# Kernel tuning notes

Hardware: AMD Instinct MI355X
Metric: run time of the kernel (lower is better)

## Reference

```python
import jax, jax.numpy as jnp
import numpy as np

NUM_HEADS = 16


def _rope_tables(seq_len, head_dim, dtype=jnp.float32):
    inv_freq = 1.0 / (10000.0 ** (jnp.arange(0, head_dim, 2, dtype=jnp.float32) / head_dim))
    t = jnp.arange(seq_len, dtype=jnp.float32)
    freqs = jnp.einsum('i,j->ij', t, inv_freq)            # [s, d/2]
    emb = jnp.concatenate([freqs, freqs], axis=-1)        # [s, d]
    return emb.astype(dtype).cos if False else (jnp.cos(emb).astype(dtype), jnp.sin(emb).astype(dtype))


def _rotate_half(x):
    x1, x2 = jnp.split(x, 2, axis=-1)
    return jnp.concatenate([-x2, x1], axis=-1)


def setup_inputs() -> dict:
    key = jax.random.key(0)
    ks = jax.random.split(key, 5)
    B, S, H = 32, 256, 2048
    hidden_states = jax.random.normal(ks[0], (B, S, H), dtype=jnp.float32)
    scale = 1.0 / np.sqrt(H)
    Wq = jax.random.normal(ks[1], (H, H), dtype=jnp.float32) * scale
    Wk = jax.random.normal(ks[2], (H, H), dtype=jnp.float32) * scale
    Wv = jax.random.normal(ks[3], (H, H), dtype=jnp.float32) * scale
    Wo = jax.random.normal(ks[4], (H, H), dtype=jnp.float32) * scale
    return {"hidden_states": hidden_states, "Wq": Wq, "Wk": Wk, "Wv": Wv, "Wo": Wo}


def reference(hidden_states, Wq, Wk, Wv, Wo):
    B, S, H = hidden_states.shape
    nh = NUM_HEADS
    hd = H // nh
    scale = hd ** (-0.5)

    # projections (nn.Linear: x @ W.T, no bias)
    q = hidden_states @ Wq.T
    k = hidden_states @ Wk.T
    v = hidden_states @ Wv.T

    # b s (h d) -> b h s d
    q = q.reshape(B, S, nh, hd).transpose(0, 2, 1, 3)
    k = k.reshape(B, S, nh, hd).transpose(0, 2, 1, 3)
    v = v.reshape(B, S, nh, hd).transpose(0, 2, 1, 3)

    cos, sin = _rope_tables(S, hd, hidden_states.dtype)   # [s, hd]
    cos = cos[None, None]                                  # [1,1,s,hd]
    sin = sin[None, None]
    q = q * cos + _rotate_half(q) * sin
    k = k * cos + _rotate_half(k) * sin

    attn = jnp.einsum('bhqd,bhkd->bhqk', q, k) * scale
    attn = jax.nn.softmax(attn, axis=-1)
    out = jnp.einsum('bhqk,bhkd->bhqd', attn, v)

    out = out.transpose(0, 2, 1, 3).reshape(B, S, H)       # b h s d -> b s (h d)
    return out @ Wo.T
```

## Files before the change

kernel.cpp:

```cpp
#include <hip/hip_runtime.h>
#include <math.h>

#define B_ 32
#define S_ 256
#define H_ 2048
#define NH_ 16
#define HD_ 128
#define M_ (B_*S_)
#define K_ H_

typedef unsigned short u16;
typedef unsigned int   u32;
typedef _Float16 half8 __attribute__((ext_vector_type(8)));
typedef __attribute__((ext_vector_type(8))) unsigned short ushort8;
typedef __attribute__((ext_vector_type(4))) float  floatx4;

typedef __attribute__((address_space(3))) u32 lds_u32;
typedef __attribute__((address_space(1))) const u32 glb_u32;

__device__ __forceinline__ u16 f2h(float f) {
    _Float16 h = (_Float16)f;
    u16 r; __builtin_memcpy(&r, &h, 2); return r;
}
__device__ __forceinline__ float h2f(u16 u) {
    _Float16 h; __builtin_memcpy(&h, &u, 2); return (float)h;
}
__device__ __forceinline__ void gll16(const u16* g, u16* l) {
    __builtin_amdgcn_global_load_lds((glb_u32*)g, (lds_u32*)l, 16, 0, 0);
}

__global__ __launch_bounds__(256) void cvt16(const float* __restrict__ x,
    u16* __restrict__ o, int n4)
{
    int i = blockIdx.x * 256 + threadIdx.x;
    if (i >= n4) return;
    float4 v = ((const float4*)x)[i];
    ((ushort4*)o)[i] = make_ushort4(f2h(v.x), f2h(v.y), f2h(v.z), f2h(v.w));
}

__global__ __launch_bounds__(512, 2) void gemm_f16(
    const u16* __restrict__ A, const u16* __restrict__ Bm,
    void* __restrict__ outv, int mode)
{
    __shared__ u16 sA[2][8192], sB[2][8192];

    const int tid  = threadIdx.x;
    const int lane = tid & 63, w = tid >> 6;
    const int wm   = w >> 2, wn = w & 3;
    const int r15  = lane & 15, quad = lane >> 4;

    const int bid = blockIdx.x;
    const int swz = (bid & 7) * 32 + (bid >> 3);
    const int bx  = swz & 7;
    const int by  = swz >> 3;

    const int srow = tid & 255;
    const int c0   = tid >> 8;
    const u16* gA = A  + (size_t)(by*256 + srow) * K_ + c0*8;
    const u16* gB = Bm + (size_t)(bx*256 + srow) * K_ + c0*8;
    const int segE = w * 512;
    const int segO = 4096 + w * 512;

    const int aBase = (quad*256 + wm*128 + r15) * 8;
    const int bBase = (quad*256 + wn*64  + r15) * 8;

    const floatx4 fzero = {0.f, 0.f, 0.f, 0.f};
    floatx4 acc[8][4];
#pragma unroll
    for (int mi = 0; mi < 8; ++mi)
#pragma unroll
        for (int ni = 0; ni < 4; ++ni) acc[mi][ni] = fzero;

#define STAGE4(nbuf) do {                                                   \
        gll16(gA,      &sA[nbuf][segE]); gll16(gA + 16, &sA[nbuf][segO]);   \
        gll16(gB,      &sB[nbuf][segE]); gll16(gB + 16, &sB[nbuf][segO]);   \
        gA += 32; gB += 32; } while (0)

    STAGE4(0);
    STAGE4(1);
    asm volatile("s_waitcnt vmcnt(4)" ::: "memory");
    __builtin_amdgcn_s_barrier();

    const int NT = K_/32;
    int cur = 0;
    for (int kt = 0; kt < NT; ++kt) {
        half8 a[8], b[4];
#pragma unroll
        for (int mi = 0; mi < 8; ++mi)
            a[mi] = *(const half8*)&sA[cur][aBase + mi*128];
#pragma unroll
        for (int ni = 0; ni < 4; ++ni)
            b[ni] = *(const half8*)&sB[cur][bBase + ni*128];

        __builtin_amdgcn_s_setprio(1);
#pragma unroll
        for (int mi = 0; mi < 4; ++mi)
#pragma unroll
            for (int ni = 0; ni < 4; ++ni)
                acc[mi][ni] = __builtin_amdgcn_mfma_f32_16x16x32_f16(a[mi], b[ni], acc[mi][ni], 0, 0, 0);
        __builtin_amdgcn_s_setprio(0);

        asm volatile("s_waitcnt lgkmcnt(0)" ::: "memory");
        __builtin_amdgcn_sched_barrier(0);
        __builtin_amdgcn_s_barrier();
        __builtin_amdgcn_sched_barrier(0);
        if (kt < NT - 2) {
            STAGE4(cur);
            __builtin_amdgcn_sched_barrier(0);
        }

        __builtin_amdgcn_s_setprio(1);
#pragma unroll
        for (int mi = 4; mi < 8; ++mi)
#pragma unroll
            for (int ni = 0; ni < 4; ++ni)
                acc[mi][ni] = __builtin_amdgcn_mfma_f32_16x16x32_f16(a[mi], b[ni], acc[mi][ni], 0, 0, 0);
        __builtin_amdgcn_s_setprio(0);

        if (kt < NT - 2)       asm volatile("s_waitcnt vmcnt(4)" ::: "memory");
        else if (kt == NT - 2) asm volatile("s_waitcnt vmcnt(0)" ::: "memory");
        if (kt < NT - 1) __builtin_amdgcn_s_barrier();
        cur ^= 1;
    }
#undef STAGE4

    if (mode == 0) {
        u16* out = (u16*)outv;
#pragma unroll
        for (int mi = 0; mi < 8; ++mi)
#pragma unroll
            for (int r = 0; r < 4; ++r) {
                int m  = by*256 + wm*128 + mi*16 + quad*4 + r;
                int bb = m >> 8, ss = m & 255;
#pragma unroll
                for (int ni = 0; ni < 4; ++ni) {
                    int n = bx*256 + wn*64 + ni*16 + r15;
                    int h = n >> 7, d = n & 127;
                    out[(((size_t)(bb*NH_ + h)) * S_ + ss) * HD_ + d] = f2h(acc[mi][ni][r]);
                }
            }
    } else {
        float* out = (float*)outv;
#pragma unroll
        for (int mi = 0; mi < 8; ++mi)
#pragma unroll
            for (int r = 0; r < 4; ++r) {
                int m = by*256 + wm*128 + mi*16 + quad*4 + r;
                size_t base = (size_t)m * H_ + bx*256 + wn*64 + r15;
#pragma unroll
                for (int ni = 0; ni < 4; ++ni)
                    out[base + ni*16] = acc[mi][ni][r];
            }
    }
}

__global__ __launch_bounds__(256) void rope_f16(u16* __restrict__ q, u16* __restrict__ k)
{
    int idx = blockIdx.x * 256 + threadIdx.x;
    u16* p = blockIdx.y ? k : q;
    int i  = idx & 63;
    int s  = (idx >> 6) & (S_ - 1);
    int bh = idx >> 14;
    size_t base = ((size_t)bh * S_ + s) * HD_;
    float f = expf((float)i * -0.14391156831212788f);
    float ang = (float)s * f;
    float c = cosf(ang), sn = sinf(ang);
    float x0 = h2f(p[base + i]), x1 = h2f(p[base + i + 64]);
    p[base + i]      = f2h(x0 * c - x1 * sn);
    p[base + i + 64] = f2h(x1 * c + x0 * sn);
}

#define SCALE 0.08838834764831845f

__global__ __launch_bounds__(256) void attn_mfma(
    const u16* __restrict__ Q, const u16* __restrict__ K, const u16* __restrict__ V,
    u16* __restrict__ O)
{
    __shared__ u16 shQK[16384];
    __shared__ u16 shV[8192];
    u16* Qs = shQK;
    u16* Ks = shQK + 8192;
    u16* Pb = shQK;

    const int tid = threadIdx.x;
    const int lane = tid & 63, w = tid >> 6;
    const int r15 = lane & 15, quad = lane >> 4;
    const int bh = blockIdx.x;
    const int q0 = blockIdx.y << 6;
    const int wq = w * 16;

    const u16* Qg = Q + ((size_t)bh * S_ + q0) * HD_;
    const u16* Kg = K + (size_t)bh * S_ * HD_;
    const u16* Vg = V + (size_t)bh * S_ * HD_;

#pragma unroll
    for (int p = 0; p < 4; ++p) {
        int task = tid + (p << 8);
        int r = task & 63, c = task >> 6;
        *(uint4*)&Qs[(c*64 + r)*8] = *(const uint4*)&Qg[(size_t)r*HD_ + c*8];
    }

    const floatx4 fzero = {0.f, 0.f, 0.f, 0.f};
    floatx4 sc[4][4];
    for (int kt = 0; kt < 4; ++kt) {
        __syncthreads();
#pragma unroll
        for (int p = 0; p < 4; ++p) {
            int task = tid + (p << 8);
            int r = task & 63, c = task >> 6;
            *(uint4*)&Ks[(c*64 + r)*8] = *(const uint4*)&Kg[(size_t)(kt*64 + r)*HD_ + c*8];
        }
        __syncthreads();
#pragma unroll
        for (int ni = 0; ni < 4; ++ni) sc[kt][ni] = fzero;
#pragma unroll
        for (int ks = 0; ks < 4; ++ks) {
            half8 a = *(const half8*)&Qs[((ks*4 + quad)*64 + wq + r15)*8];
#pragma unroll
            for (int ni = 0; ni < 4; ++ni) {
                half8 b = *(const half8*)&Ks[((ks*4 + quad)*64 + ni*16 + r15)*8];
                sc[kt][ni] = __builtin_amdgcn_mfma_f32_16x16x32_f16(a, b, sc[kt][ni], 0, 0, 0);
            }
        }
    }
    __syncthreads();

#pragma unroll
    for (int kt = 0; kt < 4; ++kt)
#pragma unroll
        for (int ni = 0; ni < 4; ++ni) sc[kt][ni] *= SCALE;

    float rinv4[4], mrow4[4];
#pragma unroll
    for (int r = 0; r < 4; ++r) {
        float m = -1e30f;
#pragma unroll
        for (int kt = 0; kt < 4; ++kt)
#pragma unroll
            for (int ni = 0; ni < 4; ++ni) m = fmaxf(m, sc[kt][ni][r]);
#pragma unroll
        for (int o = 1; o < 16; o <<= 1) m = fmaxf(m, __shfl_xor(m, o));
        mrow4[r] = m;
    }
#pragma unroll
    for (int r = 0; r < 4; ++r) {
        float ssum = 0.f;
#pragma unroll
        for (int kt = 0; kt < 4; ++kt)
#pragma unroll
            for (int ni = 0; ni < 4; ++ni) {
                float e = __expf(sc[kt][ni][r] - mrow4[r]);
                sc[kt][ni][r] = e;
                ssum += e;
            }
#pragma unroll
        for (int o = 1; o < 16; o <<= 1) ssum += __shfl_xor(ssum, o);
        rinv4[r] = 1.f / ssum;
    }
#pragma unroll
    for (int r = 0; r < 4; ++r) {
        int row = wq + quad*4 + r;
#pragma unroll
        for (int kt = 0; kt < 4; ++kt)
#pragma unroll
            for (int ni = 0; ni < 4; ++ni) {
                int col = kt*64 + ni*16 + r15;
                Pb[((col >> 3)*64 + row)*8 + (col & 7)] = f2h(sc[kt][ni][r] * rinv4[r]);
            }
    }

    floatx4 oacc[8];
#pragma unroll
    for (int di = 0; di < 8; ++di) oacc[di] = fzero;

    for (int vt = 0; vt < 4; ++vt) {
        __syncthreads();
#pragma unroll
        for (int p = 0; p < 4; ++p) {
            int task = tid + (p << 8);
            int r = task & 63, dc = task >> 6;
            ushort8 v = *(const ushort8*)&Vg[(size_t)(vt*64 + r)*HD_ + dc*8];
#pragma unroll
            for (int j = 0; j < 8; ++j)
                shV[(((r >> 3)*128) + dc*8 + j)*8 + (r & 7)] = v[j];
        }
        __syncthreads();
#pragma unroll
        for (int ks = 0; ks < 2; ++ks) {
            int colbase = vt*64 + ks*32 + quad*8;
            half8 a = *(const half8*)&Pb[((colbase >> 3)*64 + wq + r15)*8];
            int sp = ks*32 + quad*8;
#pragma unroll
            for (int di = 0; di < 8; ++di) {
                half8 b = *(const half8*)&shV[((sp >> 3)*128 + di*16 + r15)*8];
                oacc[di] = __builtin_amdgcn_mfma_f32_16x16x32_f16(a, b, oacc[di], 0, 0, 0);
            }
        }
    }

    const int brow = bh >> 4, h = bh & 15;
#pragma unroll
    for (int r = 0; r < 4; ++r) {
        size_t base = ((size_t)(brow*S_ + q0 + wq + quad*4 + r)) * H_ + h*128 + r15;
#pragma unroll
        for (int di = 0; di < 8; ++di)
            O[base + di*16] = f2h(oacc[di][r]);
    }
}

extern "C" void kernel_launch(void* const* d_in, const int* in_sizes, int n_in,
                              void* d_out, int out_size, void* d_ws, size_t ws_size,
                              hipStream_t stream)
{
    const float* X  = (const float*)d_in[0];
    const float* Wp[4] = {(const float*)d_in[1], (const float*)d_in[2],
                          (const float*)d_in[3], (const float*)d_in[4]};
    float* outp = (float*)d_out;

    char* ws = (char*)d_ws;
    u16* Xh  = (u16*)ws;
    u16* W16 = (u16*)(ws + 33554432);
    u16* Qh  = (u16*)(ws + 67108864);
    u16* Kh  = (u16*)(ws + 100663296);
    u16* Vh  = (u16*)(ws + 134217728);
    u16* Ah  = Xh;

    cvt16<<<(M_*H_/4)/256, 256, 0, stream>>>(X, Xh, M_*H_/4);
    for (int i = 0; i < 4; ++i)
        cvt16<<<(H_*H_/4)/256, 256, 0, stream>>>(Wp[i], W16 + (size_t)i*4194304, H_*H_/4);

    gemm_f16<<<256, 512, 0, stream>>>(Xh, W16 + 0*4194304, Qh, 0);
    gemm_f16<<<256, 512, 0, stream>>>(Xh, W16 + 1*4194304, Kh, 0);
    gemm_f16<<<256, 512, 0, stream>>>(Xh, W16 + 2*4194304, Vh, 0);
    rope_f16<<<dim3(32768, 2), 256, 0, stream>>>(Qh, Kh);
    attn_mfma<<<dim3(B_*NH_, 4), 256, 0, stream>>>(Qh, Kh, Vh, Ah);
    gemm_f16<<<256, 512, 0, stream>>>(Ah, W16 + 3*4194304, outp, 1);
}
```

Measured before the change: 728.7 us.

## Fuse QKV projections into one GEMM launch and triple-buffer LDS with interleaved loads

The three separate Q/K/V projection GEMMs become one launch over a concatenated 6144-wide weight (the weights are already contiguous), and the epilogue routes each column block to the Q, K or V buffer. The GEMM main loop moves from double to triple LDS buffering, splitting global-to-LDS loads into four pieces interleaved between MFMA phases, each phase separated by a barrier. This aims to cut launch overhead, fill the GPU with 768 blocks, and hide load latency better. In exchange it adds LDS use (96KB per block, which may hurt the 2-blocks-per-CU occupancy) and more barriers per iteration.

```diff
diff --git a/kernel.cpp b/kernel.cpp
--- a/kernel.cpp
+++ b/kernel.cpp
@@ -40,9 +40,9 @@
 
 __global__ __launch_bounds__(512, 2) void gemm_f16(
     const u16* __restrict__ A, const u16* __restrict__ Bm,
-    void* __restrict__ outv, int mode)
-{
-    __shared__ u16 sA[2][8192], sB[2][8192];
+    void* __restrict__ outv, int mode, int nbx)
+{
+    __shared__ u16 sA[3][8192], sB[3][8192];
 
     const int tid  = threadIdx.x;
     const int lane = tid & 63, w = tid >> 6;
@@ -50,9 +50,9 @@
     const int r15  = lane & 15, quad = lane >> 4;
 
     const int bid = blockIdx.x;
-    const int swz = (bid & 7) * 32 + (bid >> 3);
-    const int bx  = swz & 7;
-    const int by  = swz >> 3;
+    const int swz = (bid & 7) * (nbx << 2) + (bid >> 3);
+    const int by  = swz / nbx;
+    const int bx  = swz - by * nbx;
 
     const int srow = tid & 255;
     const int c0   = tid >> 8;
@@ -71,58 +71,74 @@
 #pragma unroll
         for (int ni = 0; ni < 4; ++ni) acc[mi][ni] = fzero;
 
-#define STAGE4(nbuf) do {                                                   \
-        gll16(gA,      &sA[nbuf][segE]); gll16(gA + 16, &sA[nbuf][segO]);   \
-        gll16(gB,      &sB[nbuf][segE]); gll16(gB + 16, &sB[nbuf][segO]);   \
-        gA += 32; gB += 32; } while (0)
-
-    STAGE4(0);
-    STAGE4(1);
+#define MFMA_(d, x, y) d = __builtin_amdgcn_mfma_f32_16x16x32_f16(x, y, d, 0, 0, 0)
+#define PHASE_BAR() do { __builtin_amdgcn_sched_barrier(0); \
+        __builtin_amdgcn_s_barrier(); \
+        __builtin_amdgcn_sched_barrier(0); } while (0)
+
+    gll16(gA,      &sA[0][segE]); gll16(gA + 16, &sA[0][segO]);
+    gll16(gB,      &sB[0][segE]); gll16(gB + 16, &sB[0][segO]);
+    gA += 32; gB += 32;
+    gll16(gA,      &sA[1][segE]); gll16(gA + 16, &sA[1][segO]);
+    gll16(gB,      &sB[1][segE]); gll16(gB + 16, &sB[1][segO]);
+    gA += 32; gB += 32;
     asm volatile("s_waitcnt vmcnt(4)" ::: "memory");
     __builtin_amdgcn_s_barrier();
 
     const int NT = K_/32;
-    int cur = 0;
+    int b0 = 0, b1 = 1, b2 = 2;
     for (int kt = 0; kt < NT; ++kt) {
+        const u16* pA = sA[b0]; const u16* pB = sB[b0];
+        u16* tA = sA[b2];       u16* tB = sB[b2];
+        const bool st = (kt < NT - 2);
         half8 a[8], b[4];
-#pragma unroll
-        for (int mi = 0; mi < 8; ++mi)
-            a[mi] = *(const half8*)&sA[cur][aBase + mi*128];
-#pragma unroll
-        for (int ni = 0; ni < 4; ++ni)
-            b[ni] = *(const half8*)&sB[cur][bBase + ni*128];
-
+
+#pragma unroll
+        for (int ni = 0; ni < 4; ++ni) b[ni] = *(const half8*)&pB[bBase + ni*128];
+        a[0] = *(const half8*)&pA[aBase + 0*128];
+        a[1] = *(const half8*)&pA[aBase + 1*128];
+        if (st) gll16(gA, &tA[segE]);
+        PHASE_BAR();
         __builtin_amdgcn_s_setprio(1);
 #pragma unroll
-        for (int mi = 0; mi < 4; ++mi)
-#pragma unroll
-            for (int ni = 0; ni < 4; ++ni)
-                acc[mi][ni] = __builtin_amdgcn_mfma_f32_16x16x32_f16(a[mi], b[ni], acc[mi][ni], 0, 0, 0);
+        for (int ni = 0; ni < 4; ++ni) { MFMA_(acc[0][ni], a[0], b[ni]); MFMA_(acc[1][ni], a[1], b[ni]); }
         __builtin_amdgcn_s_setprio(0);
 
-        asm volatile("s_waitcnt lgkmcnt(0)" ::: "memory");
-        __builtin_amdgcn_sched_barrier(0);
-        __builtin_amdgcn_s_barrier();
-        __builtin_amdgcn_sched_barrier(0);
-        if (kt < NT - 2) {
-            STAGE4(cur);
-            __builtin_amdgcn_sched_barrier(0);
-        }
-
+        a[2] = *(const half8*)&pA[aBase + 2*128];
+        a[3] = *(const half8*)&pA[aBase + 3*128];
+        if (st) gll16(gA + 16, &tA[segO]);
+        PHASE_BAR();
         __builtin_amdgcn_s_setprio(1);
 #pragma unroll
-        for (int mi = 4; mi < 8; ++mi)
-#pragma unroll
-            for (int ni = 0; ni < 4; ++ni)
-                acc[mi][ni] = __builtin_amdgcn_mfma_f32_16x16x32_f16(a[mi], b[ni], acc[mi][ni], 0, 0, 0);
+        for (int ni = 0; ni < 4; ++ni) { MFMA_(acc[2][ni], a[2], b[ni]); MFMA_(acc[3][ni], a[3], b[ni]); }
+        __builtin_amdgcn_s_setprio(0);
+
+        a[4] = *(const half8*)&pA[aBase + 4*128];
+        a[5] = *(const half8*)&pA[aBase + 5*128];
+        if (st) gll16(gB, &tB[segE]);
+        PHASE_BAR();
+        __builtin_amdgcn_s_setprio(1);
+#pragma unroll
+        for (int ni = 0; ni < 4; ++ni) { MFMA_(acc[4][ni], a[4], b[ni]); MFMA_(acc[5][ni], a[5], b[ni]); }
+        __builtin_amdgcn_s_setprio(0);
+
+        a[6] = *(const half8*)&pA[aBase + 6*128];
+        a[7] = *(const half8*)&pA[aBase + 7*128];
+        if (st) gll16(gB + 16, &tB[segO]);
+        PHASE_BAR();
+        __builtin_amdgcn_s_setprio(1);
+#pragma unroll
+        for (int ni = 0; ni < 4; ++ni) { MFMA_(acc[6][ni], a[6], b[ni]); MFMA_(acc[7][ni], a[7], b[ni]); }
         __builtin_amdgcn_s_setprio(0);
 
         if (kt < NT - 2)       asm volatile("s_waitcnt vmcnt(4)" ::: "memory");
         else if (kt == NT - 2) asm volatile("s_waitcnt vmcnt(0)" ::: "memory");
-        if (kt < NT - 1) __builtin_amdgcn_s_barrier();
-        cur ^= 1;
-    }
-#undef STAGE4
+        PHASE_BAR();
+        gA += 32; gB += 32;
+        int t = b0; b0 = b1; b1 = b2; b2 = t;
+    }
+#undef MFMA_
+#undef PHASE_BAR
 
     if (mode == 0) {
         u16* out = (u16*)outv;
@@ -135,8 +151,10 @@
 #pragma unroll
                 for (int ni = 0; ni < 4; ++ni) {
                     int n = bx*256 + wn*64 + ni*16 + r15;
-                    int h = n >> 7, d = n & 127;
-                    out[(((size_t)(bb*NH_ + h)) * S_ + ss) * HD_ + d] = f2h(acc[mi][ni][r]);
+                    int which = n >> 11, rem = n & 2047;
+                    int h = rem >> 7, d = rem & 127;
+                    out[(size_t)which*16777216 +
+                        (((size_t)(bb*NH_ + h)) * S_ + ss) * HD_ + d] = f2h(acc[mi][ni][r]);
                 }
             }
     } else {
@@ -329,10 +347,8 @@
     for (int i = 0; i < 4; ++i)
         cvt16<<<(H_*H_/4)/256, 256, 0, stream>>>(Wp[i], W16 + (size_t)i*4194304, H_*H_/4);
 
-    gemm_f16<<<256, 512, 0, stream>>>(Xh, W16 + 0*4194304, Qh, 0);
-    gemm_f16<<<256, 512, 0, stream>>>(Xh, W16 + 1*4194304, Kh, 0);
-    gemm_f16<<<256, 512, 0, stream>>>(Xh, W16 + 2*4194304, Vh, 0);
+    gemm_f16<<<768, 512, 0, stream>>>(Xh, W16, Qh, 0, 24);
     rope_f16<<<dim3(32768, 2), 256, 0, stream>>>(Qh, Kh);
     attn_mfma<<<dim3(B_*NH_, 4), 256, 0, stream>>>(Qh, Kh, Vh, Ah);
-    gemm_f16<<<256, 512, 0, stream>>>(Ah, W16 + 3*4194304, outp, 1);
-}
+    gemm_f16<<<256, 512, 0, stream>>>(Ah, W16 + 3*4194304, outp, 1, 8);
+}
```

Result: faster. 641.8 us (-11.9%).
